# Performance work log

Measured on AMD Instinct MI355X. Metric: run time of the kernel, lower is better.

## Reference

```python
import jax, jax.numpy as jnp
import numpy as np

SCALE = 10.0
THRESH = 1e-3   # nn.Threshold(eps, 0)
NORM_EPS = 1e-12  # F.normalize default eps
LEAKY_SLOPE = 0.01


def _proj(x, W1, W2):
    # x: [B, C, L]; conv1x1 == channel matmul
    h = jnp.einsum('oc,bcl->bol', W1, x)
    h = jnp.where(h >= 0, h, LEAKY_SLOPE * h)
    return jnp.einsum('oc,bcl->bol', W2, h)


def _l2norm(x):
    # normalize over channel dim (dim=1), torch F.normalize semantics
    n = jnp.sqrt(jnp.sum(x * x, axis=1, keepdims=True))
    return x / jnp.maximum(n, NORM_EPS)


def setup_inputs() -> dict:
    key = jax.random.key(0)
    k1, k2, k3, k4 = jax.random.split(key, 4)
    B, C, L, OUT = 4, 64, 4096, 64
    query = jax.random.normal(k1, (B, C, L), dtype=jnp.float32)
    kv = jax.random.normal(k2, (B, C, L), dtype=jnp.float32)
    W1 = jax.random.normal(k3, (2 * C, C), dtype=jnp.float32) * (1.0 / np.sqrt(C))
    W2 = jax.random.normal(k4, (OUT, 2 * C), dtype=jnp.float32) * (1.0 / np.sqrt(2 * C))
    return {"query": query, "key": kv, "W1": W1, "W2": W2}


def reference(query, key, W1, W2):
    # self_attention=True: query_conv is key_conv (shared weights)
    q = _l2norm(_proj(query, W1, W2))   # [B, O, L]
    k = _l2norm(_proj(key, W1, W2))     # [B, O, L]
    scores = jnp.einsum('bcl,bcm->blm', q, k) * SCALE  # [B, L, L]
    w = jax.nn.softmax(scores, axis=-1)
    return jnp.where(w > THRESH, w, 0.0)
```

## Files before the change

kernel.cpp:

```cpp
#include <hip/hip_runtime.h>
#include <math.h>

#define B 4
#define C 64
#define L 4096
#define OUTC 64
#define SCALE 10.0f
#define THRESH 1e-3f

typedef float v4f __attribute__((ext_vector_type(4)));
typedef short bf16x8 __attribute__((ext_vector_type(8)));
typedef unsigned short us8 __attribute__((ext_vector_type(8)));

__device__ __forceinline__ unsigned short f2bf(float x) {
    unsigned int u = __float_as_uint(x);
    u += 0x7fffu + ((u >> 16) & 1u);
    return (unsigned short)(u >> 16);
}
__device__ __forceinline__ float bf2f(unsigned short h) {
    return __uint_as_float(((unsigned int)h) << 16);
}
__device__ __forceinline__ v4f mfma16(bf16x8 a, bf16x8 b, v4f c) {
    return __builtin_amdgcn_mfma_f32_16x16x32_bf16(a, b, c, 0, 0, 0);
}


__global__ void __launch_bounds__(256) proj_kernel(
    const float* __restrict__ q_in, const float* __restrict__ k_in,
    const float* __restrict__ W1, const float* __restrict__ W2,
    unsigned short* __restrict__ Qh, unsigned short* __restrict__ Ql,
    unsigned short* __restrict__ Kh, unsigned short* __restrict__ Kl)
{
    int bid   = blockIdx.x;
    int xcd   = bid & 7;
    int b     = xcd >> 1;
    int which = (bid >> 3) & 1;
    int lt    = ((bid >> 4) << 1) | (xcd & 1);
    int l0    = lt << 6;
    int t     = threadIdx.x;
    int g     = t >> 6;
    int l     = t & 63;

    const float* __restrict__ src =
        (which ? k_in : q_in) + (size_t)b * C * L + l0 + l;
    unsigned short* __restrict__ dh = which ? Kh : Qh;
    unsigned short* __restrict__ dl = which ? Kl : Ql;

    __shared__ float Ht[128][65];
    __shared__ float red[4][64];

    float xr[C];
    #pragma unroll
    for (int c = 0; c < C; ++c)
        xr[c] = src[(size_t)c * L];

    #pragma unroll 1
    for (int oo = 0; oo < 32; oo += 4) {
        #pragma unroll
        for (int u = 0; u < 4; ++u) {
            int o = g * 32 + oo + u;
            float h0 = 0.f, h1 = 0.f, h2 = 0.f, h3 = 0.f;
            #pragma unroll
            for (int c = 0; c < C; c += 4) {
                h0 = fmaf(W1[o * C + c + 0], xr[c + 0], h0);
                h1 = fmaf(W1[o * C + c + 1], xr[c + 1], h1);
                h2 = fmaf(W1[o * C + c + 2], xr[c + 2], h2);
                h3 = fmaf(W1[o * C + c + 3], xr[c + 3], h3);
            }
            float h = (h0 + h1) + (h2 + h3);
            Ht[o][l] = (h >= 0.0f) ? h : 0.01f * h;
        }
    }
    __syncthreads();

    float y[16];
    #pragma unroll
    for (int u = 0; u < 16; ++u) y[u] = 0.f;

    #pragma unroll 1
    for (int hh = 0; hh < 2 * C; hh += 16) {
        float hr[16];
        #pragma unroll
        for (int r = 0; r < 16; ++r)
            hr[r] = Ht[hh + r][l];
        #pragma unroll
        for (int u = 0; u < 16; ++u) {
            int o = g * 16 + u;
            #pragma unroll
            for (int h = 0; h < 16; ++h)
                y[u] = fmaf(W2[o * (2 * C) + hh + h], hr[h], y[u]);
        }
    }

    float ss = 0.f;
    #pragma unroll
    for (int u = 0; u < 16; ++u) ss = fmaf(y[u], y[u], ss);
    red[g][l] = ss;
    __syncthreads();
    float tot = red[0][l] + red[1][l] + red[2][l] + red[3][l];
    float inv = 1.0f / fmaxf(sqrtf(tot), 1e-12f);

    unsigned short hs[16], ls[16];
    #pragma unroll
    for (int u = 0; u < 16; ++u) {
        float val = y[u] * inv;
        hs[u] = f2bf(val);
        ls[u] = f2bf(val - bf2f(hs[u]));
    }
    {
        int col   = l0 + l;
        int tile  = col >> 4;
        int lnn   = col & 15;
        int chunk = g >> 1;
        int quad0 = (g & 1) * 2;
        size_t base0 = (((size_t)b * 256 + tile) * 2 + chunk) * 512
                     + (size_t)(quad0 * 16 + lnn) * 8;
        size_t base1 = base0 + 128;
        *(us8*)(dh + base0) = *(us8*)&hs[0];
        *(us8*)(dh + base1) = *(us8*)&hs[8];
        *(us8*)(dl + base0) = *(us8*)&ls[0];
        *(us8*)(dl + base1) = *(us8*)&ls[8];
    }
}

__global__ void __launch_bounds__(512) scores_kernel(
    const unsigned short* __restrict__ Qh, const unsigned short* __restrict__ Ql,
    const unsigned short* __restrict__ Kh, const unsigned short* __restrict__ Kl,
    float* __restrict__ out)
{
    int bid  = blockIdx.x;
    int xcd  = bid & 7;
    int b    = xcd >> 1;
    int r0   = (((bid >> 3) << 1) | (xcd & 1)) << 4;
    int t    = threadIdx.x;
    int wave = t >> 6;
    int lane = t & 63;
    int quad = lane >> 4;
    int ln   = lane & 15;

    bf16x8 aQ[2][2];
    {
        size_t rowtile = (size_t)b * 256 + (r0 >> 4);
        #pragma unroll
        for (int c0 = 0; c0 < 2; ++c0) {
            size_t base = (rowtile * 2 + c0) * 512 + (size_t)lane * 8;
            aQ[c0][0] = *(const bf16x8*)(Qh + base);
            aQ[c0][1] = *(const bf16x8*)(Ql + base);
        }
    }

    const size_t ktb = (size_t)b * 256;
    __shared__ float wsum[16][8];
    __shared__ float rinv[16];
    __shared__ float Pt[2][16][132];

    float e[32][4];
    v4f ps = (v4f){0.f, 0.f, 0.f, 0.f};

    #pragma unroll
    for (int i = 0; i < 32; ++i) {
        size_t base = ((ktb + i * 8 + wave) * 2) * 512 + (size_t)lane * 8;
        bf16x8 bh0 = *(const bf16x8*)(Kh + base);
        bf16x8 bl0 = *(const bf16x8*)(Kl + base);
        bf16x8 bh1 = *(const bf16x8*)(Kh + base + 512);
        bf16x8 bl1 = *(const bf16x8*)(Kl + base + 512);

        v4f acc = (v4f){0.f, 0.f, 0.f, 0.f};
        acc = mfma16(aQ[0][0], bh0, acc);
        acc = mfma16(aQ[0][1], bh0, acc);
        acc = mfma16(aQ[0][0], bl0, acc);
        acc = mfma16(aQ[1][0], bh1, acc);
        acc = mfma16(aQ[1][1], bh1, acc);
        acc = mfma16(aQ[1][0], bl1, acc);
        #pragma unroll
        for (int r = 0; r < 4; ++r) {
            float ev = __expf(fmaf(SCALE, acc[r], -SCALE));
            e[i][r] = ev;
            ps[r] += ev;
        }
    }

    #pragma unroll
    for (int r = 0; r < 4; ++r) {
        float s = ps[r];
        s += __shfl_xor(s, 1);
        s += __shfl_xor(s, 2);
        s += __shfl_xor(s, 4);
        s += __shfl_xor(s, 8);
        if (ln == 0) wsum[quad * 4 + r][wave] = s;
    }
    __syncthreads();
    if (t < 16) {
        float s = 0.f;
        #pragma unroll
        for (int w = 0; w < 8; ++w) s += wsum[t][w];
        rinv[t] = 1.0f / s;
    }
    __syncthreads();

    float rv[4];
    #pragma unroll
    for (int r = 0; r < 4; ++r)
        rv[r] = rinv[quad * 4 + r];

    float* __restrict__ outb = out + ((size_t)b * L + r0) * L;
    int srow = t >> 5;
    int scol = (t & 31) * 4;

    #pragma unroll
    for (int T = 0; T < 32; ++T) {
        int buf = T & 1;
        #pragma unroll
        for (int r = 0; r < 4; ++r) {
            float w = e[T][r] * rv[r];
            w = (w > THRESH) ? w : 0.f;
            Pt[buf][quad * 4 + r][wave * 16 + ln] = w;
        }
        __syncthreads();

        v4f o = *(const v4f*)&Pt[buf][srow][scol];
        __builtin_nontemporal_store(
            o, (v4f*)(outb + (size_t)srow * L + T * 128 + scol));
    }
}

extern "C" void kernel_launch(void* const* d_in, const int* in_sizes, int n_in,
                              void* d_out, int out_size, void* d_ws, size_t ws_size,
                              hipStream_t stream) {
    const float* query = (const float*)d_in[0];
    const float* key   = (const float*)d_in[1];
    const float* W1    = (const float*)d_in[2];
    const float* W2    = (const float*)d_in[3];
    float* out = (float*)d_out;

    unsigned short* Qh = (unsigned short*)d_ws;
    unsigned short* Ql = Qh + (size_t)B * L * OUTC;
    unsigned short* Kh = Ql + (size_t)B * L * OUTC;
    unsigned short* Kl = Kh + (size_t)B * L * OUTC;

    hipLaunchKernelGGL(proj_kernel, dim3(512), dim3(256), 0, stream,
                       query, key, W1, W2, Qh, Ql, Kh, Kl);
    hipLaunchKernelGGL(scores_kernel, dim3(1024), dim3(512), 0, stream,
                       Qh, Ql, Kh, Kl, out);
}
```

Before: 382.5 us.

## Stage exp scores in fp16 shared memory instead of registers; double-buffer K loads

The scores kernel no longer keeps all 128 exp values per thread in registers. It stores them as fp16 in a 131 KB dynamic shared buffer, then writes the normalized, thresholded output row-wise with a single loop and no per-tile barriers. K tile loads are double-buffered in a non-unrolled loop. The intent is to cut register pressure and remove 32 syncthreads. The cost is large LDS use (one block per CU), added fp16 rounding of the exp values before the threshold compare, and the missing error checking that a dynamic shared size above 64 KB may need.

New measurement: 377.0 us. No clear change (-1.4%).

```diff
diff --git a/kernel.cpp b/kernel.cpp
--- a/kernel.cpp
+++ b/kernel.cpp
@@ -8,9 +8,16 @@
 #define SCALE 10.0f
 #define THRESH 1e-3f
 
+#define EROW 4100
+#define SMEM_E_BYTES (16 * EROW * 2)
+#define SMEM_WSUM_OFF SMEM_E_BYTES
+#define SMEM_RINV_OFF (SMEM_E_BYTES + 512)
+#define SMEM_BYTES (SMEM_E_BYTES + 512 + 64)
+
 typedef float v4f __attribute__((ext_vector_type(4)));
 typedef short bf16x8 __attribute__((ext_vector_type(8)));
 typedef unsigned short us8 __attribute__((ext_vector_type(8)));
+typedef unsigned short us4 __attribute__((ext_vector_type(4)));
 
 __device__ __forceinline__ unsigned short f2bf(float x) {
     unsigned int u = __float_as_uint(x);
@@ -123,11 +130,24 @@
     }
 }
 
+#define LOADK(SET, TILE) do {                                            \
+    size_t _kb = ((ktb + (size_t)(TILE)) * 2) * 512 + (size_t)lane * 8;  \
+    SET##h0 = *(const bf16x8*)(Kh + _kb);                                \
+    SET##l0 = *(const bf16x8*)(Kl + _kb);                                \
+    SET##h1 = *(const bf16x8*)(Kh + _kb + 512);                          \
+    SET##l1 = *(const bf16x8*)(Kl + _kb + 512);                          \
+} while (0)
+
 __global__ void __launch_bounds__(512) scores_kernel(
     const unsigned short* __restrict__ Qh, const unsigned short* __restrict__ Ql,
     const unsigned short* __restrict__ Kh, const unsigned short* __restrict__ Kl,
     float* __restrict__ out)
 {
+    extern __shared__ unsigned char smem[];
+    unsigned short* __restrict__ e_t  = (unsigned short*)smem;
+    float*          __restrict__ wsum = (float*)(smem + SMEM_WSUM_OFF);
+    float*          __restrict__ rinv = (float*)(smem + SMEM_RINV_OFF);
+
     int bid  = blockIdx.x;
     int xcd  = bid & 7;
     int b    = xcd >> 1;
@@ -137,6 +157,8 @@
     int lane = t & 63;
     int quad = lane >> 4;
     int ln   = lane & 15;
+    int wave16ln = wave * 16 + ln;
+    int rowbase  = quad * 4;
 
     bf16x8 aQ[2][2];
     {
@@ -150,34 +172,35 @@
     }
 
     const size_t ktb = (size_t)b * 256;
-    __shared__ float wsum[16][8];
-    __shared__ float rinv[16];
-    __shared__ float Pt[2][16][132];
-
-    float e[32][4];
+
     v4f ps = (v4f){0.f, 0.f, 0.f, 0.f};
-
-    #pragma unroll
-    for (int i = 0; i < 32; ++i) {
-        size_t base = ((ktb + i * 8 + wave) * 2) * 512 + (size_t)lane * 8;
-        bf16x8 bh0 = *(const bf16x8*)(Kh + base);
-        bf16x8 bl0 = *(const bf16x8*)(Kl + base);
-        bf16x8 bh1 = *(const bf16x8*)(Kh + base + 512);
-        bf16x8 bl1 = *(const bf16x8*)(Kl + base + 512);
-
-        v4f acc = (v4f){0.f, 0.f, 0.f, 0.f};
-        acc = mfma16(aQ[0][0], bh0, acc);
-        acc = mfma16(aQ[0][1], bh0, acc);
-        acc = mfma16(aQ[0][0], bl0, acc);
-        acc = mfma16(aQ[1][0], bh1, acc);
-        acc = mfma16(aQ[1][1], bh1, acc);
-        acc = mfma16(aQ[1][0], bl1, acc);
-        #pragma unroll
-        for (int r = 0; r < 4; ++r) {
-            float ev = __expf(fmaf(SCALE, acc[r], -SCALE));
-            e[i][r] = ev;
-            ps[r] += ev;
-        }
+    bf16x8 Ah0, Al0, Ah1, Al1, Bh0, Bl0, Bh1, Bl1;
+
+#define P1TILE(SET, COL0) do {                                           \
+    v4f acc = (v4f){0.f, 0.f, 0.f, 0.f};                                 \
+    acc = mfma16(aQ[0][0], SET##h0, acc);                                \
+    acc = mfma16(aQ[0][1], SET##h0, acc);                                \
+    acc = mfma16(aQ[0][0], SET##l0, acc);                                \
+    acc = mfma16(aQ[1][0], SET##h1, acc);                                \
+    acc = mfma16(aQ[1][1], SET##h1, acc);                                \
+    acc = mfma16(aQ[1][0], SET##l1, acc);                                \
+    _Pragma("unroll")                                                    \
+    for (int r = 0; r < 4; ++r) {                                        \
+        float ev = __expf(fmaf(SCALE, acc[r], -SCALE));                  \
+        ps[r] += ev;                                                     \
+        e_t[(rowbase + r) * EROW + (COL0) + wave16ln] =                  \
+            __builtin_bit_cast(unsigned short, (_Float16)ev);            \
+    }                                                                    \
+} while (0)
+
+    LOADK(A, wave);
+    #pragma unroll 1
+    for (int i = 0; i < 32; i += 2) {
+        LOADK(B, (i + 1) * 8 + wave);
+        P1TILE(A, i * 128);
+        if (i + 2 < 32)
+            LOADK(A, (i + 2) * 8 + wave);
+        P1TILE(B, (i + 1) * 128);
     }
 
     #pragma unroll
@@ -187,40 +210,38 @@
         s += __shfl_xor(s, 2);
         s += __shfl_xor(s, 4);
         s += __shfl_xor(s, 8);
-        if (ln == 0) wsum[quad * 4 + r][wave] = s;
+        if (ln == 0) wsum[(rowbase + r) * 8 + wave] = s;
     }
     __syncthreads();
     if (t < 16) {
         float s = 0.f;
         #pragma unroll
-        for (int w = 0; w < 8; ++w) s += wsum[t][w];
+        for (int w = 0; w < 8; ++w) s += wsum[t * 8 + w];
         rinv[t] = 1.0f / s;
     }
     __syncthreads();
 
-    float rv[4];
-    #pragma unroll
-    for (int r = 0; r < 4; ++r)
-        rv[r] = rinv[quad * 4 + r];
-
-    float* __restrict__ outb = out + ((size_t)b * L + r0) * L;
-    int srow = t >> 5;
-    int scol = (t & 31) * 4;
-
-    #pragma unroll
-    for (int T = 0; T < 32; ++T) {
-        int buf = T & 1;
-        #pragma unroll
-        for (int r = 0; r < 4; ++r) {
-            float w = e[T][r] * rv[r];
-            w = (w > THRESH) ? w : 0.f;
-            Pt[buf][quad * 4 + r][wave * 16 + ln] = w;
-        }
-        __syncthreads();
-
-        v4f o = *(const v4f*)&Pt[buf][srow][scol];
-        __builtin_nontemporal_store(
-            o, (v4f*)(outb + (size_t)srow * L + T * 128 + scol));
+    {
+        float* __restrict__ outb = out + ((size_t)b * L + r0) * L;
+        int row = t >> 5;
+        int c0  = (t & 31) * 4;
+        float ri = rinv[row];
+        const unsigned short* __restrict__ erow = e_t + (size_t)row * EROW;
+        float* __restrict__ orow = outb + (size_t)row * L;
+
+        #pragma unroll 4
+        for (int it = 0; it < 32; ++it) {
+            int col = it * 128 + c0;
+            us4 hv = *(const us4*)(erow + col);
+            v4f o;
+            #pragma unroll
+            for (int j = 0; j < 4; ++j) {
+                float w = (float)__builtin_bit_cast(_Float16,
+                                                    (unsigned short)hv[j]) * ri;
+                o[j] = (w > THRESH) ? w : 0.f;
+            }
+            __builtin_nontemporal_store(o, (v4f*)(orow + col));
+        }
     }
 }
 
@@ -240,6 +261,6 @@
 
     hipLaunchKernelGGL(proj_kernel, dim3(512), dim3(256), 0, stream,
                        query, key, W1, W2, Qh, Ql, Kh, Kl);
-    hipLaunchKernelGGL(scores_kernel, dim3(1024), dim3(512), 0, stream,
+    hipLaunchKernelGGL(scores_kernel, dim3(1024), dim3(512), SMEM_BYTES, stream,
                        Qh, Ql, Kh, Kl, out);
 }
```
